# Performance work log

Measured on AMD Instinct MI355X. Metric: run time of the kernel, lower is better.

The kernel has to match this reference:

```python
import jax, jax.numpy as jnp
import numpy as np

# Dims: B=8, C=64, H=W=256. 1x1 conv QKV projections (channel-mixing matmuls).

def setup_inputs() -> dict:
    key = jax.random.key(0)
    ks = jax.random.split(key, 7)
    B, C, H, W = 8, 64, 256, 256
    scale = 1.0 / np.sqrt(C)
    x = jax.random.normal(ks[0], (B, C, H, W), dtype=jnp.float32)
    wq = jax.random.normal(ks[1], (C, C), dtype=jnp.float32) * scale
    bq = jax.random.normal(ks[2], (C,), dtype=jnp.float32) * 0.01
    wk = jax.random.normal(ks[3], (C, C), dtype=jnp.float32) * scale
    bk = jax.random.normal(ks[4], (C,), dtype=jnp.float32) * 0.01
    wv = jax.random.normal(ks[5], (C, C), dtype=jnp.float32) * scale
    bv = jax.random.normal(ks[6], (C,), dtype=jnp.float32) * 0.01
    gamma = jnp.full((1,), 2.0, dtype=jnp.float32)  # nn.Parameter(FloatTensor([2]))
    return {"x": x, "wq": wq, "bq": bq, "wk": wk, "bk": bk, "wv": wv, "bv": bv, "gamma": gamma}


def reference(x, wq, bq, wk, bk, wv, bv, gamma):
    # 1x1 convs == per-pixel channel mixing
    Q = jnp.einsum('bchw,oc->bohw', x, wq) + bq[None, :, None, None]
    K = jnp.einsum('bchw,oc->bohw', x, wk) + bk[None, :, None, None]
    V = jnp.einsum('bchw,oc->bohw', x, wv) + bv[None, :, None, None]
    g = jax.nn.sigmoid(gamma)[0]  # sigmoid(2.0) > 0, eye-bias always applied
    # att[b,c,h,g] = sum_w Q[b,c,h,w] * K[b,c,g,w]  (key transposed on dims 2,3)
    att = jnp.einsum('bchw,bcgw->bchg', Q, K)
    H = att.shape[2]
    att = att + g * jnp.eye(H, dtype=att.dtype)
    # NOTE: softmax over the QUERY axis (dim=2), faithful to torch source
    att = jax.nn.softmax(att, axis=2)
    out = jnp.einsum('bchg,bcgw->bchw', att, V)
    return out
```

## Files before the change

kernel.cpp:

```cpp
#include <hip/hip_runtime.h>

typedef _Float16 f16x8 __attribute__((ext_vector_type(8)));
typedef _Float16 f16x4 __attribute__((ext_vector_type(4)));
typedef float    f32x4 __attribute__((ext_vector_type(4)));
typedef unsigned int u32x4 __attribute__((ext_vector_type(4)));

__device__ __forceinline__ void lds_barrier() {
    asm volatile("s_waitcnt lgkmcnt(0)" ::: "memory");
    __builtin_amdgcn_sched_barrier(0);
    __builtin_amdgcn_s_barrier();
    __builtin_amdgcn_sched_barrier(0);
}

#define W_OFF   0
#define XA_OFF  24576
#define XB_OFF  40960
#define OUT_OFF 57344

__global__ __launch_bounds__(256, 2) void proj_qkv_mfma(
    const float* __restrict__ x,
    const float* __restrict__ wq, const float* __restrict__ bq,
    const float* __restrict__ wk, const float* __restrict__ bk,
    const float* __restrict__ wv, const float* __restrict__ bv,
    _Float16* __restrict__ Qh, _Float16* __restrict__ Kh, _Float16* __restrict__ Vh,
    const int rstride)
{
    __shared__ __align__(16) unsigned char lds[81920];

    const int tid  = threadIdx.x;
    const int lane = tid & 63;
    const int wid  = tid >> 6;
    const int q4   = lane >> 4;
    const int l15  = lane & 15;

    const int pg0  = blockIdx.x << 10;
    const int bb   = pg0 >> 16;
    const int pix0 = pg0 & 65535;
    const float* xb = x + ((size_t)bb << 22);

    const int sc = tid >> 5;
    const int sslot = tid & 31;

    float bld[12];
#pragma unroll
    for (int ot = 0; ot < 12; ++ot) {
        const int mat = ot >> 2;
        const float* bs = (mat == 0) ? bq : (mat == 1) ? bk : bv;
        bld[ot] = bs[((ot & 3) << 4) + l15];
    }

#pragma unroll
    for (int it = 0; it < 12; ++it) {
        const int idx  = (it << 8) + tid;
        const int orow = idx >> 4;
        const int s    = idx & 15;
        const int mat  = orow >> 6;
        const float* wsrc = (mat == 0) ? wq : (mat == 1) ? wk : wv;
        const f32x4 v = *(const f32x4*)(wsrc + ((orow & 63) << 6) + (s << 2));
        f16x4 h;
#pragma unroll
        for (int j = 0; j < 4; ++j) h[j] = (_Float16)v[j];
        const int a = ((orow << 7) + (s << 3)) ^ ((orow & 7) << 4);
        *(f16x4*)(lds + W_OFF + a) = h;
    }

    {
        f32x4 xv[8];
#pragma unroll
        for (int it = 0; it < 8; ++it) {
            const int c = (it << 3) + sc;
            xv[it] = *(const f32x4*)(xb + ((size_t)c << 16) + pix0 + (sslot << 2));
        }
#pragma unroll
        for (int it = 0; it < 8; ++it) {
            const int c = (it << 3) + sc;
            f16x4 h;
#pragma unroll
            for (int j = 0; j < 4; ++j) h[j] = (_Float16)xv[it][j];
            const int a = ((c << 8) + (sslot << 3)) ^ (((c >> 3) & 7) << 4);
            *(f16x4*)(lds + XA_OFF + a) = h;
        }
    }
    __syncthreads();

    const int wpx = wid << 5;

    for (int t = 0; t < 8; ++t) {
        const int bufo = (t & 1) ? XB_OFF : XA_OFF;
        const int nbufo = (t & 1) ? XA_OFF : XB_OFF;
        const int pixT = pix0 + (t << 7);

        f32x4 xv[8];
        if (t < 7) {
            const int pixN = pixT + 128;
#pragma unroll
            for (int it = 0; it < 8; ++it) {
                const int c = (it << 3) + sc;
                xv[it] = *(const f32x4*)(xb + ((size_t)c << 16) + pixN + (sslot << 2));
            }
        }

        f16x8 af[2][2];
#pragma unroll
        for (int pt = 0; pt < 2; ++pt)
#pragma unroll
            for (int kc = 0; kc < 2; ++kc) {
                const int px = wpx + (pt << 4) + l15;
                f16x8 a;
#pragma unroll
                for (int j = 0; j < 8; ++j) {
                    const int c  = (kc << 5) + (q4 << 3) + j;
                    const int ad = ((c << 8) + (px << 1)) ^ (((c >> 3) & 7) << 4);
                    a[j] = *(const _Float16*)(lds + bufo + ad);
                }
                af[pt][kc] = a;
            }

#pragma unroll
        for (int rd = 0; rd < 2; ++rd) {
            if (rd) lds_barrier();
#pragma unroll
            for (int ot6 = 0; ot6 < 6; ++ot6) {
                const int ot  = rd * 6 + ot6;
                const int row = (ot << 4) + l15;
                const int rsw = (row & 7) << 4;
                const f16x8 bf0 = *(const f16x8*)(lds + W_OFF + (((row << 7) + (q4 << 4)) ^ rsw));
                const f16x8 bf1 = *(const f16x8*)(lds + W_OFF + (((row << 7) + 64 + (q4 << 4)) ^ rsw));
                const int oo  = (ot6 << 4) + l15;
                const int osw = (oo & 7) << 4;
#pragma unroll
                for (int pt = 0; pt < 2; ++pt) {
                    f32x4 acc = { bld[ot], bld[ot], bld[ot], bld[ot] };
                    acc = __builtin_amdgcn_mfma_f32_16x16x32_f16(af[pt][0], bf0, acc, 0, 0, 0);
                    acc = __builtin_amdgcn_mfma_f32_16x16x32_f16(af[pt][1], bf1, acc, 0, 0, 0);
                    f16x4 h;
#pragma unroll
                    for (int r = 0; r < 4; ++r) h[r] = (_Float16)acc[r];
                    const int px = wpx + (pt << 4) + (q4 << 2);
                    *(f16x4*)(lds + OUT_OFF + (((oo << 8) + (px << 1)) ^ osw)) = h;
                }
            }
            lds_barrier();

#pragma unroll
            for (int it = 0; it < 6; ++it) {
                const int idx = (it << 8) + tid;
                const int oo  = idx >> 4;
                const int sl  = idx & 15;
                const u32x4 vst = *(const u32x4*)(lds + OUT_OFF +
                    (((oo << 8) + (sl << 4)) ^ ((oo & 7) << 4)));
                const int ot  = rd * 6 + (oo >> 4);
                const int mat = ot >> 2;
                _Float16* ob = (mat == 0) ? Qh : (mat == 1) ? Kh : Vh;
                const int orow = ((ot & 3) << 4) + (oo & 15);
                u32x4* dst = (u32x4*)(ob + (size_t)((bb << 6) + orow) * rstride + pixT + (sl << 3));
                __builtin_nontemporal_store(vst, dst);
            }
        }

        if (t < 7) {
#pragma unroll
            for (int it = 0; it < 8; ++it) {
                const int c = (it << 3) + sc;
                f16x4 h;
#pragma unroll
                for (int j = 0; j < 4; ++j) h[j] = (_Float16)xv[it][j];
                const int a = ((c << 8) + (sslot << 3)) ^ (((c >> 3) & 7) << 4);
                *(f16x4*)(lds + nbufo + a) = h;
            }
        }
        lds_barrier();
    }
}

#define P_OFF 0
#define B_OFF 131072
#define K_OFF 147456

__global__ __launch_bounds__(1024, 4) void attn_rowsm(
    const _Float16* __restrict__ Qh, const _Float16* __restrict__ Kh,
    const _Float16* __restrict__ Vh, const float* __restrict__ gamma,
    float* __restrict__ out, const int rstride)
{
    __shared__ __align__(16) unsigned char lds[163840];

    const int tid  = threadIdx.x;
    const int lane = tid & 63;
    const int wid  = tid >> 6;
    const int wr   = wid >> 2;
    const int wc   = wid & 3;
    const int q4   = lane >> 4;
    const int l15  = lane & 15;
    const size_t qbase = (size_t)blockIdx.x * rstride;

    const f32x4 fzero = {0.f, 0.f, 0.f, 0.f};
    f32x4 acc[4][4];
#pragma unroll
    for (int i = 0; i < 4; ++i)
#pragma unroll
        for (int j = 0; j < 4; ++j) acc[i][j] = fzero;

    const int sh = tid >> 2;
    const int ss = tid & 3;
    const int soff = ((sh << 6) + (ss << 4)) ^ ((sh & 7) << 4);
    const size_t sg = qbase + (size_t)sh * 256 + ss * 8;

    auto qk_compute = [&]() {
        f16x8 bf[4];
#pragma unroll
        for (int ni = 0; ni < 4; ++ni) {
            const int g = (wc << 6) + (ni << 4) + l15;
            bf[ni] = *(const f16x8*)(lds + K_OFF + (((g << 6) + (q4 << 4)) ^ ((g & 7) << 4)));
        }
#pragma unroll
        for (int mi = 0; mi < 4; ++mi) {
            const int h = (wr << 6) + (mi << 4) + l15;
            const f16x8 afr = *(const f16x8*)(lds + B_OFF + (((h << 6) + (q4 << 4)) ^ ((h & 7) << 4)));
#pragma unroll
            for (int ni = 0; ni < 4; ++ni)
                acc[mi][ni] = __builtin_amdgcn_mfma_f32_16x16x32_f16(afr, bf[ni], acc[mi][ni], 0, 0, 0);
        }
    };

    uint4 qdA = *(const uint4*)(Qh + sg);
    uint4 kdA = *(const uint4*)(Kh + sg);
    uint4 qdB = *(const uint4*)(Qh + sg + 32);
    uint4 kdB = *(const uint4*)(Kh + sg + 32);

    for (int kc = 0; kc < 256; kc += 64) {
        lds_barrier();
        *(uint4*)(lds + B_OFF + soff) = qdA;
        *(uint4*)(lds + K_OFF + soff) = kdA;
        if (kc < 192) {
            qdA = *(const uint4*)(Qh + sg + kc + 64);
            kdA = *(const uint4*)(Kh + sg + kc + 64);
        }
        lds_barrier();
        qk_compute();

        lds_barrier();
        *(uint4*)(lds + B_OFF + soff) = qdB;
        *(uint4*)(lds + K_OFF + soff) = kdB;
        if (kc < 192) {
            qdB = *(const uint4*)(Qh + sg + kc + 96);
            kdB = *(const uint4*)(Kh + sg + kc + 96);
        }
        lds_barrier();
        qk_compute();
    }

    const int gg = tid >> 5;
    const int wo = tid & 31;
    const size_t vg = qbase + (size_t)gg * 256 + wo * 8;
    uint4 vdA = *(const uint4*)(Vh + vg);
    uint4 vdB = *(const uint4*)(Vh + vg + 32 * 256);

    const float g_sig = 1.0f / (1.0f + __expf(-gamma[0]));
    if (wr == wc) {
        const int rn = l15 - (q4 << 2);
        if (rn >= 0 && rn < 4) {
#pragma unroll
            for (int mi = 0; mi < 4; ++mi) acc[mi][mi][rn] += g_sig;
        }
    }

    float* red = (float*)(lds + B_OFF);
    float cmx[4], cinv[4];

    lds_barrier();
#pragma unroll
    for (int ni = 0; ni < 4; ++ni) {
        float m = -3.0e38f;
#pragma unroll
        for (int mi = 0; mi < 4; ++mi)
#pragma unroll
            for (int r = 0; r < 4; ++r) m = fmaxf(m, acc[mi][ni][r]);
        m = fmaxf(m, __shfl_xor(m, 16));
        m = fmaxf(m, __shfl_xor(m, 32));
        cmx[ni] = m;
        if (q4 == 0) red[wr * 256 + (wc << 6) + (ni << 4) + l15] = m;
    }
    lds_barrier();
#pragma unroll
    for (int ni = 0; ni < 4; ++ni) {
        const int col = (wc << 6) + (ni << 4) + l15;
        float m = red[col];
        m = fmaxf(m, red[256 + col]);
        m = fmaxf(m, red[512 + col]);
        m = fmaxf(m, red[768 + col]);
        cmx[ni] = m;
    }
    lds_barrier();
#pragma unroll
    for (int ni = 0; ni < 4; ++ni) {
        float s = 0.f;
#pragma unroll
        for (int mi = 0; mi < 4; ++mi)
#pragma unroll
            for (int r = 0; r < 4; ++r) {
                const float e = __expf(acc[mi][ni][r] - cmx[ni]);
                acc[mi][ni][r] = e;
                s += e;
            }
        s += __shfl_xor(s, 16);
        s += __shfl_xor(s, 32);
        if (q4 == 0) red[wr * 256 + (wc << 6) + (ni << 4) + l15] = s;
    }
    lds_barrier();
#pragma unroll
    for (int ni = 0; ni < 4; ++ni) {
        const int col = (wc << 6) + (ni << 4) + l15;
        cinv[ni] = 1.0f / (red[col] + red[256 + col] + red[512 + col] + red[768 + col]);
    }

#pragma unroll
    for (int mi = 0; mi < 4; ++mi) {
        const int hbase = (wr << 6) + (mi << 4) + (q4 << 2);
#pragma unroll
        for (int r = 0; r < 4; ++r) {
            const int h  = hbase + r;
            const int hb = h << 9;
            const int sw = (h & 7) << 4;
#pragma unroll
            for (int ni = 0; ni < 4; ++ni) {
                const int g = (wc << 6) + (ni << 4) + l15;
                *(_Float16*)(lds + P_OFF + ((hb + (g << 1)) ^ sw)) =
                    (_Float16)(acc[mi][ni][r] * cinv[ni]);
            }
        }
    }

#pragma unroll
    for (int i = 0; i < 4; ++i)
#pragma unroll
        for (int j = 0; j < 4; ++j) acc[i][j] = fzero;

    auto v_write = [&](const uint4& vd) {
        const _Float16* ve = (const _Float16*)&vd;
#pragma unroll
        for (int j = 0; j < 8; ++j) {
            const int w  = (wo << 3) + j;
            const int fw = ((w & 7) ^ ((w >> 3) & 7)) << 4;
            *(_Float16*)(lds + B_OFF + (((w << 6) + (gg << 1)) ^ fw)) = ve[j];
        }
    };
    auto pv_compute = [&](int gc) {
        f16x8 bf[4];
#pragma unroll
        for (int ni = 0; ni < 4; ++ni) {
            const int w  = (wc << 6) + (ni << 4) + l15;
            const int fw = ((w & 7) ^ ((w >> 3) & 7)) << 4;
            bf[ni] = *(const f16x8*)(lds + B_OFF + (((w << 6) + (q4 << 4)) ^ fw));
        }
#pragma unroll
        for (int mi = 0; mi < 4; ++mi) {
            const int h = (wr << 6) + (mi << 4) + l15;
            const f16x8 afr = *(const f16x8*)(lds + P_OFF +
                (((h << 9) + ((gc + (q4 << 3)) << 1)) ^ ((h & 7) << 4)));
#pragma unroll
            for (int ni = 0; ni < 4; ++ni)
                acc[mi][ni] = __builtin_amdgcn_mfma_f32_16x16x32_f16(afr, bf[ni], acc[mi][ni], 0, 0, 0);
        }
    };

    for (int gc = 0; gc < 256; gc += 64) {
        lds_barrier();
        v_write(vdA);
        if (gc < 192) vdA = *(const uint4*)(Vh + vg + (size_t)(gc + 64) * 256);
        lds_barrier();
        pv_compute(gc);

        lds_barrier();
        v_write(vdB);
        if (gc < 192) vdB = *(const uint4*)(Vh + vg + (size_t)(gc + 96) * 256);
        lds_barrier();
        pv_compute(gc + 32);
    }

    float* op = out + ((size_t)blockIdx.x << 16);
#pragma unroll
    for (int pass = 0; pass < 2; ++pass) {
        lds_barrier();
#pragma unroll
        for (int mi2 = 0; mi2 < 2; ++mi2) {
            const int mi = pass * 2 + mi2;
#pragma unroll
            for (int r = 0; r < 4; ++r) {
                const int lr = (wr << 5) + (mi2 << 4) + (q4 << 2) + r;
                const int sw = (lr & 7) << 4;
#pragma unroll
                for (int ni = 0; ni < 4; ++ni) {
                    const int w = (wc << 6) + (ni << 4) + l15;
                    *(float*)(lds + P_OFF + (((lr << 10) + (w << 2)) ^ sw)) =
                        acc[mi][ni][r];
                }
            }
        }
        lds_barrier();
#pragma unroll
        for (int it = 0; it < 8; ++it) {
            const int idx = (it << 10) + tid;
            const int row = idx >> 6;
            const int sl  = idx & 63;
            const u32x4 v = *(const u32x4*)(lds + P_OFF +
                (((row << 10) + (sl << 4)) ^ ((row & 7) << 4)));
            const int h = ((row >> 5) << 6) + (pass << 5) + (row & 31);
            u32x4* dst = (u32x4*)(op + (h << 8) + (sl << 2));
            __builtin_nontemporal_store(v, dst);
        }
    }
}

extern "C" void kernel_launch(void* const* d_in, const int* in_sizes, int n_in,
                              void* d_out, int out_size, void* d_ws, size_t ws_size,
                              hipStream_t stream) {
    const float* x     = (const float*)d_in[0];
    const float* wq    = (const float*)d_in[1];
    const float* bq    = (const float*)d_in[2];
    const float* wk    = (const float*)d_in[3];
    const float* bk    = (const float*)d_in[4];
    const float* wv    = (const float*)d_in[5];
    const float* bv    = (const float*)d_in[6];
    const float* gamma = (const float*)d_in[7];
    float* out = (float*)d_out;

    int rstride = 65536 + 64;
    size_t perMat = (size_t)512 * rstride;
    if (perMat * 3 * sizeof(_Float16) > ws_size) {
        rstride = 65536;
        perMat = (size_t)512 * rstride;
    }
    _Float16* Qh = (_Float16*)d_ws;
    _Float16* Kh = Qh + perMat;
    _Float16* Vh = Kh + perMat;

    proj_qkv_mfma<<<512, 256, 0, stream>>>(x, wq, bq, wk, bk, wv, bv, Qh, Kh, Vh, rstride);
    attn_rowsm<<<512, 1024, 0, stream>>>(Qh, Kh, Vh, gamma, out, rstride);
}
```

Baseline: 148.3 us.

## Stream Q/K tiles via async global-to-LDS loads with double buffering

The QK^T phase now fetches Q and K chunks with global_load_lds directly into double-buffered LDS regions, each chunk covering 64 columns, and uses vmcnt waits in place of register staging. The PV phase packs pairs of V rows into 32-bit LDS writes and processes 64-wide chunks, halving the barrier count per loop. The P-matrix swizzle changes to suit the new read pattern. This aims to cut register pressure, barriers and LDS store instructions, but it relies on the DMA wait counts and the new swizzles being correct.

```diff
diff --git a/kernel.cpp b/kernel.cpp
--- a/kernel.cpp
+++ b/kernel.cpp
@@ -4,6 +4,9 @@
 typedef _Float16 f16x4 __attribute__((ext_vector_type(4)));
 typedef float    f32x4 __attribute__((ext_vector_type(4)));
 typedef unsigned int u32x4 __attribute__((ext_vector_type(4)));
+
+typedef const __attribute__((address_space(1))) void gvoid_t;
+typedef __attribute__((address_space(3))) void lvoid_t;
 
 __device__ __forceinline__ void lds_barrier() {
     asm volatile("s_waitcnt lgkmcnt(0)" ::: "memory");
@@ -173,9 +176,9 @@
     }
 }
 
-#define P_OFF 0
-#define B_OFF 131072
-#define K_OFF 147456
+#define P_OFF  0
+#define RED_OFF 131072
+#define VT_OFF 131072
 
 __global__ __launch_bounds__(1024, 4) void attn_rowsm(
     const _Float16* __restrict__ Qh, const _Float16* __restrict__ Kh,
@@ -200,60 +203,62 @@
 #pragma unroll
         for (int j = 0; j < 4; ++j) acc[i][j] = fzero;
 
-    const int sh = tid >> 2;
-    const int ss = tid & 3;
-    const int soff = ((sh << 6) + (ss << 4)) ^ ((sh & 7) << 4);
-    const size_t sg = qbase + (size_t)sh * 256 + ss * 8;
-
-    auto qk_compute = [&]() {
-        f16x8 bf[4];
-#pragma unroll
-        for (int ni = 0; ni < 4; ++ni) {
-            const int g = (wc << 6) + (ni << 4) + l15;
-            bf[ni] = *(const f16x8*)(lds + K_OFF + (((g << 6) + (q4 << 4)) ^ ((g & 7) << 4)));
-        }
-#pragma unroll
-        for (int mi = 0; mi < 4; ++mi) {
-            const int h = (wr << 6) + (mi << 4) + l15;
-            const f16x8 afr = *(const f16x8*)(lds + B_OFF + (((h << 6) + (q4 << 4)) ^ ((h & 7) << 4)));
-#pragma unroll
-            for (int ni = 0; ni < 4; ++ni)
-                acc[mi][ni] = __builtin_amdgcn_mfma_f32_16x16x32_f16(afr, bf[ni], acc[mi][ni], 0, 0, 0);
+    auto dma_chunk = [&](int buf, int c) {
+#pragma unroll
+        for (int i = 0; i < 2; ++i) {
+            const int idx = (((wid << 1) + i) << 10);
+            const int h   = (idx >> 7) + (lane >> 3);
+            const int sl  = lane & 7;
+            const int kin = (sl << 3) ^ ((h & 7) << 3);
+            const size_t src = qbase + (size_t)h * 256 + c * 64 + kin;
+            __builtin_amdgcn_global_load_lds((gvoid_t*)(Qh + src),
+                (lvoid_t*)(lds + buf + idx), 16, 0, 0);
+            __builtin_amdgcn_global_load_lds((gvoid_t*)(Kh + src),
+                (lvoid_t*)(lds + buf + 32768 + idx), 16, 0, 0);
         }
     };
-
-    uint4 qdA = *(const uint4*)(Qh + sg);
-    uint4 kdA = *(const uint4*)(Kh + sg);
-    uint4 qdB = *(const uint4*)(Qh + sg + 32);
-    uint4 kdB = *(const uint4*)(Kh + sg + 32);
-
-    for (int kc = 0; kc < 256; kc += 64) {
-        lds_barrier();
-        *(uint4*)(lds + B_OFF + soff) = qdA;
-        *(uint4*)(lds + K_OFF + soff) = kdA;
-        if (kc < 192) {
-            qdA = *(const uint4*)(Qh + sg + kc + 64);
-            kdA = *(const uint4*)(Kh + sg + kc + 64);
-        }
-        lds_barrier();
-        qk_compute();
-
-        lds_barrier();
-        *(uint4*)(lds + B_OFF + soff) = qdB;
-        *(uint4*)(lds + K_OFF + soff) = kdB;
-        if (kc < 192) {
-            qdB = *(const uint4*)(Qh + sg + kc + 96);
-            kdB = *(const uint4*)(Kh + sg + kc + 96);
-        }
-        lds_barrier();
-        qk_compute();
-    }
-
-    const int gg = tid >> 5;
+    auto qk_chunk = [&](int buf) {
+#pragma unroll
+        for (int sub = 0; sub < 2; ++sub) {
+            f16x8 bf[4];
+#pragma unroll
+            for (int ni = 0; ni < 4; ++ni) {
+                const int g = (wc << 6) + (ni << 4) + l15;
+                bf[ni] = *(const f16x8*)(lds + buf + 32768 + (g << 7) +
+                         (((sub << 6) + (q4 << 4)) ^ ((g & 7) << 4)));
+            }
+#pragma unroll
+            for (int mi = 0; mi < 4; ++mi) {
+                const int h = (wr << 6) + (mi << 4) + l15;
+                const f16x8 afr = *(const f16x8*)(lds + buf + (h << 7) +
+                         (((sub << 6) + (q4 << 4)) ^ ((h & 7) << 4)));
+#pragma unroll
+                for (int ni = 0; ni < 4; ++ni)
+                    acc[mi][ni] = __builtin_amdgcn_mfma_f32_16x16x32_f16(afr, bf[ni], acc[mi][ni], 0, 0, 0);
+            }
+        }
+    };
+
+    dma_chunk(0, 0);
+    __builtin_amdgcn_sched_barrier(0);
+#pragma unroll
+    for (int c = 0; c < 4; ++c) {
+        const int buf  = (c & 1) << 16;
+        const int nbuf = ((c + 1) & 1) << 16;
+        if (c < 3) dma_chunk(nbuf, c + 1);
+        __builtin_amdgcn_sched_barrier(0);
+        if (c < 3) { asm volatile("s_waitcnt vmcnt(4)" ::: "memory"); }
+        else       { asm volatile("s_waitcnt vmcnt(0)" ::: "memory"); }
+        __builtin_amdgcn_sched_barrier(0);
+        lds_barrier();
+        qk_chunk(buf);
+        lds_barrier();
+    }
+
+    const int gp = tid >> 5;
     const int wo = tid & 31;
-    const size_t vg = qbase + (size_t)gg * 256 + wo * 8;
-    uint4 vdA = *(const uint4*)(Vh + vg);
-    uint4 vdB = *(const uint4*)(Vh + vg + 32 * 256);
+    uint4 vd0 = *(const uint4*)(Vh + qbase + (size_t)(gp << 1) * 256 + wo * 8);
+    uint4 vd1 = *(const uint4*)(Vh + qbase + (size_t)((gp << 1) + 1) * 256 + wo * 8);
 
     const float g_sig = 1.0f / (1.0f + __expf(-gamma[0]));
     if (wr == wc) {
@@ -264,7 +269,7 @@
         }
     }
 
-    float* red = (float*)(lds + B_OFF);
+    float* red = (float*)(lds + RED_OFF);
     float cmx[4], cinv[4];
 
     lds_barrier();
@@ -320,7 +325,7 @@
         for (int r = 0; r < 4; ++r) {
             const int h  = hbase + r;
             const int hb = h << 9;
-            const int sw = (h & 7) << 4;
+            const int sw = ((h & 3) << 4) ^ (((h >> 2) & 3) << 5);
 #pragma unroll
             for (int ni = 0; ni < 4; ++ni) {
                 const int g = (wc << 6) + (ni << 4) + l15;
@@ -335,46 +340,51 @@
 #pragma unroll
         for (int j = 0; j < 4; ++j) acc[i][j] = fzero;
 
-    auto v_write = [&](const uint4& vd) {
-        const _Float16* ve = (const _Float16*)&vd;
+    auto v_scatter = [&](const uint4& a, const uint4& b) {
+        const unsigned short* e0 = (const unsigned short*)&a;
+        const unsigned short* e1 = (const unsigned short*)&b;
 #pragma unroll
         for (int j = 0; j < 8; ++j) {
             const int w  = (wo << 3) + j;
             const int fw = ((w & 7) ^ ((w >> 3) & 7)) << 4;
-            *(_Float16*)(lds + B_OFF + (((w << 6) + (gg << 1)) ^ fw)) = ve[j];
+            const unsigned int pk = (unsigned int)e0[j] | ((unsigned int)e1[j] << 16);
+            *(unsigned int*)(lds + VT_OFF + (((w << 7) + (gp << 2)) ^ fw)) = pk;
         }
     };
-    auto pv_compute = [&](int gc) {
-        f16x8 bf[4];
-#pragma unroll
-        for (int ni = 0; ni < 4; ++ni) {
-            const int w  = (wc << 6) + (ni << 4) + l15;
-            const int fw = ((w & 7) ^ ((w >> 3) & 7)) << 4;
-            bf[ni] = *(const f16x8*)(lds + B_OFF + (((w << 6) + (q4 << 4)) ^ fw));
-        }
-#pragma unroll
-        for (int mi = 0; mi < 4; ++mi) {
-            const int h = (wr << 6) + (mi << 4) + l15;
-            const f16x8 afr = *(const f16x8*)(lds + P_OFF +
-                (((h << 9) + ((gc + (q4 << 3)) << 1)) ^ ((h & 7) << 4)));
-#pragma unroll
-            for (int ni = 0; ni < 4; ++ni)
-                acc[mi][ni] = __builtin_amdgcn_mfma_f32_16x16x32_f16(afr, bf[ni], acc[mi][ni], 0, 0, 0);
+    auto pv_chunk = [&](int gc) {
+#pragma unroll
+        for (int sub = 0; sub < 2; ++sub) {
+            f16x8 bf[4];
+#pragma unroll
+            for (int ni = 0; ni < 4; ++ni) {
+                const int w  = (wc << 6) + (ni << 4) + l15;
+                const int fw = ((w & 7) ^ ((w >> 3) & 7)) << 4;
+                bf[ni] = *(const f16x8*)(lds + VT_OFF + (w << 7) +
+                         (((sub << 6) + (q4 << 4)) ^ fw));
+            }
+#pragma unroll
+            for (int mi = 0; mi < 4; ++mi) {
+                const int h  = (wr << 6) + (mi << 4) + l15;
+                const int sw = ((h & 3) << 4) ^ (((h >> 2) & 3) << 5);
+                const f16x8 afr = *(const f16x8*)(lds + P_OFF + (h << 9) +
+                    ((((gc + (sub << 5) + (q4 << 3)) << 1)) ^ sw));
+#pragma unroll
+                for (int ni = 0; ni < 4; ++ni)
+                    acc[mi][ni] = __builtin_amdgcn_mfma_f32_16x16x32_f16(afr, bf[ni], acc[mi][ni], 0, 0, 0);
+            }
         }
     };
 
     for (int gc = 0; gc < 256; gc += 64) {
         lds_barrier();
-        v_write(vdA);
-        if (gc < 192) vdA = *(const uint4*)(Vh + vg + (size_t)(gc + 64) * 256);
-        lds_barrier();
-        pv_compute(gc);
-
-        lds_barrier();
-        v_write(vdB);
-        if (gc < 192) vdB = *(const uint4*)(Vh + vg + (size_t)(gc + 96) * 256);
-        lds_barrier();
-        pv_compute(gc + 32);
+        v_scatter(vd0, vd1);
+        if (gc < 192) {
+            const size_t vgn = qbase + (size_t)(gc + 64 + (gp << 1)) * 256 + wo * 8;
+            vd0 = *(const uint4*)(Vh + vgn);
+            vd1 = *(const uint4*)(Vh + vgn + 256);
+        }
+        lds_barrier();
+        pv_chunk(gc);
     }
 
     float* op = out + ((size_t)blockIdx.x << 16);
```

After: 146.1 us. No clear change (-1.5%).
